# Kernel optimization log

Hardware: AMD Instinct MI355X
Metric: run time of the kernel (lower is better)

The kernel has to match this reference:

```python
import jax, jax.numpy as jnp
import numpy as np


def setup_inputs() -> dict:
    key = jax.random.key(0)
    k1, k2 = jax.random.split(key)
    B, N, D = 32, 576, 1024  # CLIP ViT-L/14: 24x24 patches, width 1024
    hidden_states = jax.random.normal(k1, (B, N + 1, D), dtype=jnp.float32)
    cls_attn = jax.random.uniform(k2, (B, N), dtype=jnp.float32)
    return {"hidden_states": hidden_states, "cls_attn": cls_attn, "dominant_num": 128}


def scope_select(feats, cls_attn, num_selected):
    """Greedy coverage-maximizing token selection (SCOPE), batched.
    feats: [B, N, D], cls_attn: [B, N]. Returns selected indices [B, K].
    ALPHA=1.0 and COMBINED='multi' (the defaults in the source).
    """
    norm = feats / jnp.linalg.norm(feats, axis=-1, keepdims=True)
    sim = jnp.einsum('bnd,bmd->bnm', norm, norm)  # [B, N, N]
    B, N = feats.shape[0], feats.shape[1]
    batch_ix = jnp.arange(B)

    def step(carry, _):
        selected, cur_max = carry  # [B, N] bool, [B, N] float
        # zero out already-selected candidate columns j, then coverage gain
        masked = jnp.where(selected[:, None, :], 0.0, sim)  # [B, i, j]
        gains = jnp.maximum(masked - cur_max[:, :, None], 0.0).sum(axis=1)  # [B, N]
        gains = gains * cls_attn  # combined='multi', alpha=1.0
        gains = jnp.where(selected, -jnp.inf, gains)
        best = jnp.argmax(gains, axis=1)  # [B]
        selected = selected.at[batch_ix, best].set(True)
        cur_max = jnp.maximum(cur_max, sim[batch_ix, best])  # running coverage max
        return (selected, cur_max), best

    init = (jnp.zeros((B, N), dtype=bool), jnp.zeros((B, N), dtype=feats.dtype))
    _, idx = jax.lax.scan(step, init, None, length=num_selected)  # [K, B]
    return idx.T  # [B, K]


def reference(hidden_states, cls_attn, dominant_num):
    # drop CLS token (index 0) for selection
    image_features = hidden_states[:, 1:]  # [B, N, D]
    selected_idx = scope_select(image_features, cls_attn, dominant_num) + 1  # [B, K], +1 for CLS offset
    # torch masked_select preserves original index order -> gather sorted indices
    gather_idx = jnp.sort(selected_idx, axis=1)
    dominant_tokens = jnp.take_along_axis(hidden_states, gather_idx[:, :, None], axis=1)  # [B, K, D]
    return dominant_tokens, selected_idx
```

## Files before the change

kernel.cpp:

```cpp
#include <hip/hip_runtime.h>

#define BB 32
#define NN 576
#define DD 1024
#define KK 128
#define HS_N 577

__global__ __launch_bounds__(256) void norm_kernel(const float* __restrict__ hs,
                                                   float* __restrict__ inv) {
    int row = blockIdx.x;
    int b = row / NN, n = row % NN;
    const float4* p = (const float4*)(hs + ((size_t)b * HS_N + n + 1) * DD);
    int t = threadIdx.x;
    float4 v = p[t];
    double s = (double)v.x * v.x + (double)v.y * v.y + (double)v.z * v.z + (double)v.w * v.w;
    for (int off = 32; off; off >>= 1) s += __shfl_xor(s, off);
    __shared__ double wsum[4];
    int lane = t & 63, w = t >> 6;
    if (lane == 0) wsum[w] = s;
    __syncthreads();
    if (t == 0) {
        double tot = wsum[0] + wsum[1] + wsum[2] + wsum[3];
        inv[row] = 1.0f / (float)sqrt(tot);
    }
}

#define KC 16
#define LDT 68
#define TLD 68
__global__ __launch_bounds__(256) void sim_kernel(const float* __restrict__ hs,
                                                  const float* __restrict__ inv,
                                                  float* __restrict__ sim) {
    int b = blockIdx.z;
    int l = blockIdx.x;
    int ti = 0;
    while (l >= 9 - ti) { l -= 9 - ti; ti++; }
    int tj = ti + l;
    int m0 = ti * 64, n0 = tj * 64;
    const float* feats = hs + ((size_t)b * HS_N + 1) * DD;
    __shared__ float As[KC * LDT];
    __shared__ float Bs[KC * LDT];
    __shared__ float tile[64 * TLD];
    int t = threadIdx.x;
    int lrow = t >> 2, lc4 = (t & 3) << 2;
    float invA = inv[b * NN + m0 + lrow];
    float invB = inv[b * NN + n0 + lrow];
    const float* gA = feats + (size_t)(m0 + lrow) * DD + lc4;
    const float* gB = feats + (size_t)(n0 + lrow) * DD + lc4;
    int tx = t & 15, ty = t >> 4;
    float acc[4][4] = {};
    for (int k0 = 0; k0 < DD; k0 += KC) {
        float4 a = *(const float4*)(gA + k0);
        float4 bv = *(const float4*)(gB + k0);
        __syncthreads();
        As[(lc4 + 0) * LDT + lrow] = a.x * invA;
        As[(lc4 + 1) * LDT + lrow] = a.y * invA;
        As[(lc4 + 2) * LDT + lrow] = a.z * invA;
        As[(lc4 + 3) * LDT + lrow] = a.w * invA;
        Bs[(lc4 + 0) * LDT + lrow] = bv.x * invB;
        Bs[(lc4 + 1) * LDT + lrow] = bv.y * invB;
        Bs[(lc4 + 2) * LDT + lrow] = bv.z * invB;
        Bs[(lc4 + 3) * LDT + lrow] = bv.w * invB;
        __syncthreads();
#pragma unroll
        for (int kk = 0; kk < KC; kk++) {
            float4 av = *(const float4*)&As[kk * LDT + (tx << 2)];
            float4 bw = *(const float4*)&Bs[kk * LDT + (ty << 2)];
            float aa[4] = {av.x, av.y, av.z, av.w};
            float bb[4] = {bw.x, bw.y, bw.z, bw.w};
#pragma unroll
            for (int i = 0; i < 4; i++)
#pragma unroll
                for (int j = 0; j < 4; j++) acc[i][j] += aa[i] * bb[j];
        }
    }
#pragma unroll
    for (int i = 0; i < 4; i++) {
        size_t m = m0 + (tx << 2) + i;
        float4 o = {acc[i][0], acc[i][1], acc[i][2], acc[i][3]};
        *(float4*)(sim + ((size_t)b * NN + m) * NN + n0 + (ty << 2)) = o;
    }
    if (ti != tj) {
        __syncthreads();
#pragma unroll
        for (int i = 0; i < 4; i++) {
            float4 o = {acc[i][0], acc[i][1], acc[i][2], acc[i][3]};
            *(float4*)&tile[((tx << 2) + i) * TLD + (ty << 2)] = o;
        }
        __syncthreads();
#pragma unroll
        for (int r = 0; r < 4; r++) {
            int a = (tx << 2) + r;
            float4 o;
            o.x = tile[((ty << 2) + 0) * TLD + a];
            o.y = tile[((ty << 2) + 1) * TLD + a];
            o.z = tile[((ty << 2) + 2) * TLD + a];
            o.w = tile[((ty << 2) + 3) * TLD + a];
            *(float4*)(sim + ((size_t)b * NN + n0 + a) * NN + m0 + (ty << 2)) = o;
        }
    }
}

__global__ __launch_bounds__(256) void init_gain_kernel(const float* __restrict__ sim,
                                                        double* __restrict__ g0,
                                                        float* __restrict__ pad) {
    if (blockIdx.x == 0 && blockIdx.y == 0) {
        int tt = threadIdx.x;
        pad[tt] = 0.f; pad[tt + 256] = 0.f;
        if (tt < 64) pad[tt + 512] = 0.f;
    }
    int b = blockIdx.y;
    int m = (blockIdx.x << 2) + (threadIdx.x >> 6);
    int lane = threadIdx.x & 63;
    const float* row = sim + ((size_t)b * NN + m) * NN;
    double s = 0.0;
#pragma unroll
    for (int j = 0; j < 9; j++) s += (double)fmaxf(row[(j << 6) + lane], 0.f);
    for (int off = 32; off; off >>= 1) s += __shfl_xor(s, off);
    if (lane == 0) g0[b * NN + m] = s;
}

#define LOAD_BUF8(X, N4, J)                                                    \
    {                                                                          \
        int jj8 = (J) << 3;                                                    \
        int4 oa = *(const int4*)&choff[jj8];                                   \
        int4 ob = *(const int4*)&choff[jj8 + 4];                               \
        X[0] = *(const float*)(Sc + (unsigned)(oa.x + t4));                    \
        X[1] = *(const float*)(Sc + (unsigned)(oa.y + t4));                    \
        X[2] = *(const float*)(Sc + (unsigned)(oa.z + t4));                    \
        X[3] = *(const float*)(Sc + (unsigned)(oa.w + t4));                    \
        X[4] = *(const float*)(Sc + (unsigned)(ob.x + t4));                    \
        X[5] = *(const float*)(Sc + (unsigned)(ob.y + t4));                    \
        X[6] = *(const float*)(Sc + (unsigned)(ob.z + t4));                    \
        X[7] = *(const float*)(Sc + (unsigned)(ob.w + t4));                    \
        int jh = (J) << 2;                                                     \
        N4[0] = chonw4[jh + 0];                                                \
        N4[1] = chonw4[jh + 1];                                                \
        N4[2] = chonw4[jh + 2];                                                \
        N4[3] = chonw4[jh + 3];                                                \
    }

#define COMP_BUF8(X, N4)                                                       \
    {                                                                          \
        _Pragma("unroll") for (int q = 0; q < 4; q++) {                        \
            float o0 = N4[q].x, w0 = N4[q].y;                                  \
            gg += (double)(o0 - __builtin_amdgcn_fmed3f(X[2 * q], o0, w0));    \
            float o1 = N4[q].z, w1 = N4[q].w;                                  \
            gg += (double)(o1 - __builtin_amdgcn_fmed3f(X[2 * q + 1], o1, w1));\
        }                                                                      \
    }

__global__ __launch_bounds__(576, 1) void select_kernel(const float* __restrict__ sim,
                                                        const double* __restrict__ g0,
                                                        const float* __restrict__ cls,
                                                        float* __restrict__ out_idx,
                                                        int* __restrict__ gsorted) {
    int b = blockIdx.x;
    const float* S = sim + (size_t)b * NN * NN;
    const char* Sc = (const char*)S;
    int t = threadIdx.x, lane = t & 63, w = t >> 6;
    const int t4 = t << 2;
    __shared__ float2 ovnw[NN];
    __shared__ int    choff[NN + 8];
    __shared__ float4 chonw4[(NN + 8) / 2];
    __shared__ unsigned long long chmask[9];
    __shared__ double rv[9];
    __shared__ int    ri[9];
    __shared__ float  selseq[KK];
    __shared__ int    wcnt[9];
    float2* chonw = (float2*)chonw4;

    double gg = g0[b * NN + t];
    double cl = (double)cls[b * NN + t];
    float mycmax = 0.f;
    bool sel = false;
    const int c0 = t;

    for (int k = 0; k < KK; k++) {
        if (k > 0) {
            int pos = 0;
#pragma unroll
            for (int q = 0; q < 9; q++) {
                unsigned long long m = chmask[q];
                if ((m >> lane) & 1ull) {
                    int col = (q << 6) + lane;
                    int p = pos + __popcll(m & ((1ull << lane) - 1ull));
                    choff[p] = col * 2304;
                    chonw[p] = ovnw[col];
                }
                pos += __popcll(m);
            }
            int cc = pos;
            int padc = (8 - (cc & 7)) & 7;
            if (lane < padc) {
                choff[cc + lane] = NN * 2304;
                chonw[cc + lane] = make_float2(0.f, 0.f);
            }
            int nbat = (cc + padc) >> 3;

            float xA[8]; float4 nA[4];
            float xB[8]; float4 nB[4];
            LOAD_BUF8(xA, nA, 0);
            for (int j = 0; j < nbat; ) {
                int jn = (j + 1 < nbat) ? j + 1 : j;
                LOAD_BUF8(xB, nB, jn);
                __builtin_amdgcn_sched_barrier(0);
                COMP_BUF8(xA, nA);
                j++;
                if (j >= nbat) break;
                jn = (j + 1 < nbat) ? j + 1 : j;
                LOAD_BUF8(xA, nA, jn);
                __builtin_amdgcn_sched_barrier(0);
                COMP_BUF8(xB, nB);
                j++;
            }
        }
        double v = sel ? -1.0 : gg * cl;
        int idx = c0;
        for (int off = 32; off; off >>= 1) {
            double ov = __shfl_xor(v, off);
            int oi = __shfl_xor(idx, off);
            if (ov > v || (ov == v && oi < idx)) { v = ov; idx = oi; }
        }
        if (lane == 0) { rv[w] = v; ri[w] = idx; }
        __syncthreads();
        double bv = rv[0]; int mstar = ri[0];
#pragma unroll
        for (int q = 1; q < 9; q++) {
            double qv = rv[q]; int qi = ri[q];
            if (qv > bv || (qv == bv && qi < mstar)) { bv = qv; mstar = qi; }
        }
        float s0 = S[(size_t)mstar * NN + t];
        float o0 = mycmax, n0 = fmaxf(o0, s0);
        bool h0 = n0 > o0;
        unsigned long long m0 = __ballot(h0);
        ovnw[c0] = make_float2(o0, n0); mycmax = n0;
        if (lane == 0) chmask[w] = m0;
        if (c0 == mstar) { sel = true; selseq[k] = (float)(mstar + 1); }
        __syncthreads();
    }

    if (t < KK) out_idx[b * KK + t] = selseq[t];
    unsigned long long mk = __ballot(sel);
    if (lane == 0) wcnt[w] = __popcll(mk);
    __syncthreads();
    int r = __popcll(mk & ((1ull << lane) - 1));
    int pre = 0;
#pragma unroll
    for (int q = 0; q < 9; q++) if (q < w) pre += wcnt[q];
    if (sel) gsorted[b * KK + pre + r] = c0 + 1;
}

__global__ __launch_bounds__(256) void gather_kernel(const float* __restrict__ hs,
                                                     const int* __restrict__ gsorted,
                                                     float* __restrict__ out) {
    int blk = blockIdx.x;
    int b = blk >> 7, j = blk & 127;
    int row = gsorted[b * KK + j];
    const float4* src = (const float4*)(hs + ((size_t)b * HS_N + row) * DD);
    float4* dst = (float4*)(out + ((size_t)b * KK + j) * DD);
    dst[threadIdx.x] = src[threadIdx.x];
}

extern "C" void kernel_launch(void* const* d_in, const int* in_sizes, int n_in,
                              void* d_out, int out_size, void* d_ws, size_t ws_size,
                              hipStream_t stream) {
    const float* hs = (const float*)d_in[0];
    const float* cls = (const float*)d_in[1];
    float* sim = (float*)d_ws;
    float* pad = sim + (size_t)BB * NN * NN;
    char* xregion = (char*)(pad + NN);
    float* inv = (float*)xregion;
    double* g0 = (double*)xregion;
    int* gsorted = (int*)(xregion + (size_t)BB * NN * sizeof(double));
    float* out_tokens = (float*)d_out;
    float* out_idx = out_tokens + (size_t)BB * KK * DD;

    norm_kernel<<<BB * NN, 256, 0, stream>>>(hs, inv);
    sim_kernel<<<dim3(45, 1, BB), 256, 0, stream>>>(hs, inv, sim);
    init_gain_kernel<<<dim3(NN / 4, BB), 256, 0, stream>>>(sim, g0, pad);
    select_kernel<<<BB, 576, 0, stream>>>(sim, g0, cls, out_idx, gsorted);
    gather_kernel<<<BB * KK, 256, 0, stream>>>(hs, gsorted, out_tokens);
}
```

Baseline: 724.5 us.

## Double-buffer sim GEMM shared tiles and triple-buffer greedy selection loads

The similarity GEMM now uses a larger K chunk with two shared-memory buffers and register prefetch of the next chunk. This removes one barrier per iteration and overlaps global loads with the FMAs. The greedy selection inner loop moves from double to triple buffering, so loads run two batches ahead of compute. The cost is higher register and LDS pressure, which may reduce occupancy.

```diff
diff --git a/kernel.cpp b/kernel.cpp
--- a/kernel.cpp
+++ b/kernel.cpp
@@ -25,7 +25,7 @@
     }
 }
 
-#define KC 16
+#define KC 32
 #define LDT 68
 #define TLD 68
 __global__ __launch_bounds__(256) void sim_kernel(const float* __restrict__ hs,
@@ -38,34 +38,52 @@
     int tj = ti + l;
     int m0 = ti * 64, n0 = tj * 64;
     const float* feats = hs + ((size_t)b * HS_N + 1) * DD;
-    __shared__ float As[KC * LDT];
-    __shared__ float Bs[KC * LDT];
+    __shared__ float As[2][KC * LDT];
+    __shared__ float Bs[2][KC * LDT];
     __shared__ float tile[64 * TLD];
     int t = threadIdx.x;
-    int lrow = t >> 2, lc4 = (t & 3) << 2;
+    int lrow = t >> 2, lc8 = (t & 3) << 3;
     float invA = inv[b * NN + m0 + lrow];
     float invB = inv[b * NN + n0 + lrow];
-    const float* gA = feats + (size_t)(m0 + lrow) * DD + lc4;
-    const float* gB = feats + (size_t)(n0 + lrow) * DD + lc4;
+    const float* gA = feats + (size_t)(m0 + lrow) * DD + lc8;
+    const float* gB = feats + (size_t)(n0 + lrow) * DD + lc8;
     int tx = t & 15, ty = t >> 4;
     float acc[4][4] = {};
+    float4 a0 = *(const float4*)(gA);
+    float4 a1 = *(const float4*)(gA + 4);
+    float4 b0 = *(const float4*)(gB);
+    float4 b1 = *(const float4*)(gB + 4);
+    int cur = 0;
     for (int k0 = 0; k0 < DD; k0 += KC) {
-        float4 a = *(const float4*)(gA + k0);
-        float4 bv = *(const float4*)(gB + k0);
-        __syncthreads();
-        As[(lc4 + 0) * LDT + lrow] = a.x * invA;
-        As[(lc4 + 1) * LDT + lrow] = a.y * invA;
-        As[(lc4 + 2) * LDT + lrow] = a.z * invA;
-        As[(lc4 + 3) * LDT + lrow] = a.w * invA;
-        Bs[(lc4 + 0) * LDT + lrow] = bv.x * invB;
-        Bs[(lc4 + 1) * LDT + lrow] = bv.y * invB;
-        Bs[(lc4 + 2) * LDT + lrow] = bv.z * invB;
-        Bs[(lc4 + 3) * LDT + lrow] = bv.w * invB;
-        __syncthreads();
+        float* Ac = As[cur];
+        float* Bc = Bs[cur];
+        Ac[(lc8 + 0) * LDT + lrow] = a0.x * invA;
+        Ac[(lc8 + 1) * LDT + lrow] = a0.y * invA;
+        Ac[(lc8 + 2) * LDT + lrow] = a0.z * invA;
+        Ac[(lc8 + 3) * LDT + lrow] = a0.w * invA;
+        Ac[(lc8 + 4) * LDT + lrow] = a1.x * invA;
+        Ac[(lc8 + 5) * LDT + lrow] = a1.y * invA;
+        Ac[(lc8 + 6) * LDT + lrow] = a1.z * invA;
+        Ac[(lc8 + 7) * LDT + lrow] = a1.w * invA;
+        Bc[(lc8 + 0) * LDT + lrow] = b0.x * invB;
+        Bc[(lc8 + 1) * LDT + lrow] = b0.y * invB;
+        Bc[(lc8 + 2) * LDT + lrow] = b0.z * invB;
+        Bc[(lc8 + 3) * LDT + lrow] = b0.w * invB;
+        Bc[(lc8 + 4) * LDT + lrow] = b1.x * invB;
+        Bc[(lc8 + 5) * LDT + lrow] = b1.y * invB;
+        Bc[(lc8 + 6) * LDT + lrow] = b1.z * invB;
+        Bc[(lc8 + 7) * LDT + lrow] = b1.w * invB;
+        __syncthreads();
+        if (k0 + KC < DD) {
+            a0 = *(const float4*)(gA + k0 + KC);
+            a1 = *(const float4*)(gA + k0 + KC + 4);
+            b0 = *(const float4*)(gB + k0 + KC);
+            b1 = *(const float4*)(gB + k0 + KC + 4);
+        }
 #pragma unroll
         for (int kk = 0; kk < KC; kk++) {
-            float4 av = *(const float4*)&As[kk * LDT + (tx << 2)];
-            float4 bw = *(const float4*)&Bs[kk * LDT + (ty << 2)];
+            float4 av = *(const float4*)&Ac[kk * LDT + (tx << 2)];
+            float4 bw = *(const float4*)&Bc[kk * LDT + (ty << 2)];
             float aa[4] = {av.x, av.y, av.z, av.w};
             float bb[4] = {bw.x, bw.y, bw.z, bw.w};
 #pragma unroll
@@ -73,6 +91,7 @@
 #pragma unroll
                 for (int j = 0; j < 4; j++) acc[i][j] += aa[i] * bb[j];
         }
+        cur ^= 1;
     }
 #pragma unroll
     for (int i = 0; i < 4; i++) {
@@ -200,18 +219,23 @@
 
             float xA[8]; float4 nA[4];
             float xB[8]; float4 nB[4];
+            float xC[8]; float4 nC[4];
             LOAD_BUF8(xA, nA, 0);
+            if (nbat > 1) LOAD_BUF8(xB, nB, 1);
             for (int j = 0; j < nbat; ) {
-                int jn = (j + 1 < nbat) ? j + 1 : j;
-                LOAD_BUF8(xB, nB, jn);
+                if (j + 2 < nbat) LOAD_BUF8(xC, nC, j + 2);
                 __builtin_amdgcn_sched_barrier(0);
                 COMP_BUF8(xA, nA);
                 j++;
                 if (j >= nbat) break;
-                jn = (j + 1 < nbat) ? j + 1 : j;
-                LOAD_BUF8(xA, nA, jn);
+                if (j + 2 < nbat) LOAD_BUF8(xA, nA, j + 2);
                 __builtin_amdgcn_sched_barrier(0);
                 COMP_BUF8(xB, nB);
+                j++;
+                if (j >= nbat) break;
+                if (j + 2 < nbat) LOAD_BUF8(xB, nB, j + 2);
+                __builtin_amdgcn_sched_barrier(0);
+                COMP_BUF8(xC, nC);
                 j++;
             }
         }
```

New measurement: 720.7 us. Within noise of the previous version (-0.5%).
